# Kernel optimization log

Measured on AMD Instinct MI355X. Metric: run time of the kernel, lower is better.

Reference implementation:

```python
import jax, jax.numpy as jnp
import numpy as np

B, N, M, K, S, P, H, W = 8, 32, 32, 3, 1, 1, 192, 192
NH = (H + 2 * P - K) // S + 1
NW = (W + 2 * P - K) // S + 1


def setup_inputs() -> dict:
    key = jax.random.key(0)
    ks = jax.random.split(key, 8)
    f = lambda k, sh, sc: jax.random.normal(k, sh, jnp.float32) * sc
    return {
        "x": f(ks[0], (B, N, H, W), 1.0),
        "a1_w": f(ks[1], (K * K, N, K, K), 0.05),  # attention1 conv k x k
        "a1_b": jnp.zeros((K * K,), jnp.float32),
        "a2_w": f(ks[2], (K * K, K * K), 0.1),      # attention1 1x1 conv
        "a2_b": jnp.zeros((K * K,), jnp.float32),
        "a3_w": f(ks[3], (K * K, K * K), 0.1),      # attention1 1x1 conv
        "a3_b": jnp.zeros((K * K,), jnp.float32),
        "b1_w": f(ks[4], (M, N), 0.05),             # attention3 1x1 conv
        "b1_b": jnp.zeros((M,), jnp.float32),
        "b2_w": f(ks[5], (M, M), 0.05),             # attention3 1x1 conv
        "b2_b": jnp.zeros((M,), jnp.float32),
        "weight": f(ks[6], (M, N, K, K), 0.05),     # main conv weight
    }


def _attention1(x, a1_w, a1_b, a2_w, a2_b, a3_w, a3_b):
    # Conv(k) -> ReLU -> Conv1x1 -> ReLU -> Conv1x1 -> Sigmoid; out [B, K*K, NH, NW]
    a = jax.lax.conv_general_dilated(
        x, a1_w, (S, S), [(P, P), (P, P)],
        dimension_numbers=("NCHW", "OIHW", "NCHW"))
    a = jax.nn.relu(a + a1_b[None, :, None, None])
    a = jax.nn.relu(jnp.einsum("oi,bihw->bohw", a2_w, a) + a2_b[None, :, None, None])
    a = jnp.einsum("oi,bihw->bohw", a3_w, a) + a3_b[None, :, None, None]
    return jax.nn.sigmoid(a)


def _unfold(x):
    # torch F.unfold ordering: channel-major, kernel positions inner.
    # returns [B, N, K*K, NH, NW]
    xp = jnp.pad(x, ((0, 0), (0, 0), (P, P), (P, P)))
    cols = [xp[:, :, i:i + (NH - 1) * S + 1:S, j:j + (NW - 1) * S + 1:S]
            for i in range(K) for j in range(K)]
    return jnp.stack(cols, axis=2)


def reference(x, a1_w, a1_b, a2_w, a2_b, a3_w, a3_b, b1_w, b1_b, b2_w, b2_b, weight):
    att = _attention1(x, a1_w, a1_b, a2_w, a2_b, a3_w, a3_b)  # [B, K*K, NH, NW]
    pat = _unfold(x)                                          # [B, N, K*K, NH, NW]
    w = weight.reshape(M, N, K * K)
    # attention-weighted unfold + matmul + fold, fused as one einsum
    y = jnp.einsum("bnphw,bphw,mnp->bmhw", pat, att, w)       # [B, M, NH, NW]
    # attention3 bias: global avg pool -> 1x1 -> ReLU -> 1x1
    pooled = x.mean(axis=(2, 3))                              # [B, N]
    h = jax.nn.relu(pooled @ b1_w.T + b1_b)
    bias = h @ b2_w.T + b2_b                                  # [B, M]
    return y + bias[:, :, None, None]
```

## Files before the change

### kernel.cpp

```cpp
#include <hip/hip_runtime.h>
#include <math.h>

#define B_ 8
#define N_ 32
#define M_ 32
#define HW 192

typedef __attribute__((ext_vector_type(8))) short short8;
typedef __attribute__((ext_vector_type(4))) float float4_;

__device__ inline unsigned short f2bf(float f) {
    unsigned int b = __float_as_uint(f);
    b += 0x7FFF + ((b >> 16) & 1);
    return (unsigned short)(b >> 16);
}
__device__ inline float bf2f(unsigned short u) {
    return __uint_as_float((unsigned int)u << 16);
}

union U8 { short8 s; unsigned int u[4]; };

__global__ __launch_bounds__(256) void pool_prep_kernel(
    const float* __restrict__ x, const float* __restrict__ a1w,
    const float* __restrict__ weight, float* __restrict__ pooled,
    unsigned short* __restrict__ a1A, unsigned short* __restrict__ wA) {
    if (blockIdx.x == 256) {
        int tid = threadIdx.x;
        for (int idx = tid; idx < 9 * 512; idx += 256) {
            int j = idx & 7, l = (idx >> 3) & 63, c = idx >> 9;
            int o = l & 15, n = (l >> 4) * 8 + j;
            float v = (o < 9) ? a1w[(o * N_ + n) * 9 + c] : 0.f;
            a1A[idx] = f2bf(v);
        }
        for (int idx = tid; idx < 9 * 1024; idx += 256) {
            int j = idx & 7, l = (idx >> 3) & 63, mt = (idx >> 9) & 1, c = idx >> 10;
            int m = mt * 16 + (l & 15), n = (l >> 4) * 8 + j;
            wA[idx] = f2bf(weight[(m * N_ + n) * 9 + c]);
        }
        return;
    }
    int bn = blockIdx.x;
    const float4_* p = (const float4_*)(x + (size_t)bn * (HW * HW));
    float s = 0.f;
    for (int i = threadIdx.x; i < (HW * HW) / 4; i += 256) {
        float4_ v = p[i];
        s += (v[0] + v[1]) + (v[2] + v[3]);
    }
#pragma unroll
    for (int off = 32; off > 0; off >>= 1) s += __shfl_down(s, off, 64);
    __shared__ float red[4];
    if ((threadIdx.x & 63) == 0) red[threadIdx.x >> 6] = s;
    __syncthreads();
    if (threadIdx.x == 0)
        pooled[bn] = (red[0] + red[1] + red[2] + red[3]) * (1.f / (HW * HW));
}

__global__ __launch_bounds__(256) void laconv_kernel(
    const float* __restrict__ x, const float* __restrict__ a1b,
    const float* __restrict__ a2w, const float* __restrict__ a2b,
    const float* __restrict__ a3w, const float* __restrict__ a3b,
    const unsigned short* __restrict__ a1A, const unsigned short* __restrict__ wA,
    const float* __restrict__ pooled, const float* __restrict__ b1w,
    const float* __restrict__ b1b, const float* __restrict__ b2w,
    const float* __restrict__ b2b, float* __restrict__ out) {
    __shared__ __align__(16) unsigned short xs[324 * 40];
    __shared__ unsigned short att_s[9 * 264];
    __shared__ float hsh[M_];
    __shared__ __align__(16) float bias_lds[M_];

    const int id = blockIdx.x;
    const int b = id & 7;
    const int t = id >> 3;
    const int bx = t % 12, by = t / 12;
    const int th0 = by * 16, tw0 = bx * 16;
    const int tid = threadIdx.x;
    const int wv = tid >> 6, lane = tid & 63;
    const int tx = lane & 15, ks = lane >> 4;
    const float* xb = x + (size_t)b * N_ * HW * HW;

    float fv[5][8];
    int posv[5], grpv[5];
#pragma unroll
    for (int it0 = 0; it0 < 5; ++it0) {
        int it = tid + it0 * 256;
        int grp = it / 324;
        int pos = it - grp * 324;
        posv[it0] = pos; grpv[it0] = grp;
        int r = pos / 18, cc = pos - r * 18;
        int h = th0 + r - 1, wc = tw0 + cc - 1;
        const float* src = xb + (size_t)(grp * 8) * (HW * HW) + h * HW + wc;
        if (((unsigned)h < HW) && ((unsigned)wc < HW)) {
#pragma unroll
            for (int i = 0; i < 8; ++i) fv[it0][i] = src[i * (HW * HW)];
        } else {
#pragma unroll
            for (int i = 0; i < 8; ++i) fv[it0][i] = 0.f;
        }
    }
    float fr[8];
    int posr = 0;
    if (tid < 16) {
        int it = 1280 + tid;
        int pos = it - 3 * 324;
        posr = pos;
        int r = pos / 18, cc = pos - r * 18;
        int h = th0 + r - 1, wc = tw0 + cc - 1;
        const float* src = xb + (size_t)24 * (HW * HW) + h * HW + wc;
        if (((unsigned)h < HW) && ((unsigned)wc < HW)) {
#pragma unroll
            for (int i = 0; i < 8; ++i) fr[i] = src[i * (HW * HW)];
        } else {
#pragma unroll
            for (int i = 0; i < 8; ++i) fr[i] = 0.f;
        }
    }
#pragma unroll
    for (int it0 = 0; it0 < 5; ++it0) {
        U8 tt;
#pragma unroll
        for (int i = 0; i < 4; ++i)
            tt.u[i] = (unsigned)f2bf(fv[it0][2 * i]) |
                      ((unsigned)f2bf(fv[it0][2 * i + 1]) << 16);
        *(short8*)&xs[posv[it0] * 40 + grpv[it0] * 8] = tt.s;
    }
    if (tid < 16) {
        U8 tt;
#pragma unroll
        for (int i = 0; i < 4; ++i)
            tt.u[i] = (unsigned)f2bf(fr[2 * i]) | ((unsigned)f2bf(fr[2 * i + 1]) << 16);
        *(short8*)&xs[posr * 40 + 24] = tt.s;
    }
    if (tid < M_) {
        float s = b1b[tid];
#pragma unroll
        for (int n = 0; n < N_; n++) s += pooled[b * N_ + n] * b1w[tid * N_ + n];
        hsh[tid] = fmaxf(s, 0.f);
    }
    __syncthreads();
    if (tid < M_) {
        float s2 = b2b[tid];
#pragma unroll
        for (int q = 0; q < M_; q++) s2 += hsh[q] * b2w[tid * M_ + q];
        bias_lds[tid] = s2;
    }

    const int pb = (wv * 4) * 720 + tx * 40 + ks * 8;
    const float4_ zero4 = {0.f, 0.f, 0.f, 0.f};

    float4_ aacc[4];
#pragma unroll
    for (int g = 0; g < 4; ++g) aacc[g] = zero4;
#pragma unroll
    for (int c = 0; c < 9; ++c) {
        short8 aA = ((const short8*)a1A)[c * 64 + lane];
        const int coff = (c / 3) * 720 + (c % 3) * 40;
#pragma unroll
        for (int g = 0; g < 4; ++g) {
            short8 bP = *(const short8*)&xs[pb + g * 720 + coff];
            aacc[g] = __builtin_amdgcn_mfma_f32_16x16x32_bf16(aA, bP, aacc[g], 0, 0, 0);
        }
    }
#pragma unroll
    for (int g = 0; g < 4; ++g) {
#pragma unroll
        for (int reg = 0; reg < 4; ++reg) {
            int o = ks * 4 + reg;
            if (o < 9) att_s[o * 264 + (wv * 4 + g) * 16 + tx] = f2bf(aacc[g][reg]);
        }
    }
    __syncthreads();

    float t1[9], t2[9], attv[9];
#pragma unroll
    for (int o = 0; o < 9; ++o)
        t1[o] = fmaxf(bf2f(att_s[o * 264 + tid]) + a1b[o], 0.f);
#pragma unroll
    for (int o2 = 0; o2 < 9; ++o2) {
        float s = a2b[o2];
#pragma unroll
        for (int o = 0; o < 9; ++o) s += a2w[o2 * 9 + o] * t1[o];
        t2[o2] = fmaxf(s, 0.f);
    }
#pragma unroll
    for (int o3 = 0; o3 < 9; ++o3) {
        float s = a3b[o3];
#pragma unroll
        for (int o2 = 0; o2 < 9; ++o2) s += a3w[o3 * 9 + o2] * t2[o2];
        attv[o3] = 1.f / (1.f + __expf(-s));
    }
#pragma unroll
    for (int p = 0; p < 9; ++p) att_s[p * 264 + tid] = f2bf(attv[p]);
    __syncthreads();

    float4_ acc0[4], acc1[4];
#pragma unroll
    for (int g = 0; g < 4; ++g) { acc0[g] = zero4; acc1[g] = zero4; }
#pragma unroll
    for (int c = 0; c < 9; ++c) {
        short8 w0 = ((const short8*)wA)[c * 128 + lane];
        short8 w1 = ((const short8*)wA)[c * 128 + 64 + lane];
        const int coff = (c / 3) * 720 + (c % 3) * 40;
#pragma unroll
        for (int g = 0; g < 4; ++g) {
            short8 bP = *(const short8*)&xs[pb + g * 720 + coff];
            float av = bf2f(att_s[c * 264 + (wv * 4 + g) * 16 + tx]);
            float4_ av4 = {av, av, av, av};
            float4_ z0 = __builtin_amdgcn_mfma_f32_16x16x32_bf16(w0, bP, zero4, 0, 0, 0);
            float4_ z1 = __builtin_amdgcn_mfma_f32_16x16x32_bf16(w1, bP, zero4, 0, 0, 0);
            acc0[g] = acc0[g] + av4 * z0;
            acc1[g] = acc1[g] + av4 * z1;
        }
    }

    const int wc = tw0 + tx;
    float4_ bv0 = *(const float4_*)&bias_lds[ks * 4];
    float4_ bv1 = *(const float4_*)&bias_lds[16 + ks * 4];
#pragma unroll
    for (int g = 0; g < 4; ++g) {
        int h = th0 + wv * 4 + g;
#pragma unroll
        for (int reg = 0; reg < 4; ++reg) {
            int m0 = ks * 4 + reg;
            out[((b * M_ + m0) * HW + h) * HW + wc] = acc0[g][reg] + bv0[reg];
            out[((b * M_ + m0 + 16) * HW + h) * HW + wc] = acc1[g][reg] + bv1[reg];
        }
    }
}

extern "C" void kernel_launch(void* const* d_in, const int* in_sizes, int n_in,
                              void* d_out, int out_size, void* d_ws,
                              size_t ws_size, hipStream_t stream) {
    const float* x   = (const float*)d_in[0];
    const float* a1w = (const float*)d_in[1];
    const float* a1b = (const float*)d_in[2];
    const float* a2w = (const float*)d_in[3];
    const float* a2b = (const float*)d_in[4];
    const float* a3w = (const float*)d_in[5];
    const float* a3b = (const float*)d_in[6];
    const float* b1w = (const float*)d_in[7];
    const float* b1b = (const float*)d_in[8];
    const float* b2w = (const float*)d_in[9];
    const float* b2b = (const float*)d_in[10];
    const float* wgt = (const float*)d_in[11];
    float* out = (float*)d_out;

    char* ws = (char*)d_ws;
    float* pooled        = (float*)(ws);
    unsigned short* a1A  = (unsigned short*)(ws + 2048);
    unsigned short* wAf  = (unsigned short*)(ws + 11264);

    pool_prep_kernel<<<dim3(B_ * N_ + 1), dim3(256), 0, stream>>>(
        x, a1w, wgt, pooled, a1A, wAf);
    laconv_kernel<<<dim3(12 * 12 * B_), dim3(256), 0, stream>>>(
        x, a1b, a2w, a2b, a3w, a3b, a1A, wAf, pooled, b1w, b1b, b2w, b2b, out);
    (void)in_sizes; (void)n_in; (void)out_size; (void)ws_size;
}
```

Measured before the change: 145.0 us.

## Pre-convert input to channels-last bf16 buffer before main conv kernel

```diff
diff --git a/kernel.cpp b/kernel.cpp
--- a/kernel.cpp
+++ b/kernel.cpp
@@ -5,6 +5,9 @@
 #define N_ 32
 #define M_ 32
 #define HW 192
+#define NPIX (HW * HW)
+#define CONV_BLKS (B_ * 144)
+#define POOL_BLKS (B_ * N_)
 
 typedef __attribute__((ext_vector_type(8))) short short8;
 typedef __attribute__((ext_vector_type(4))) float float4_;
@@ -20,43 +23,64 @@
 
 union U8 { short8 s; unsigned int u[4]; };
 
-__global__ __launch_bounds__(256) void pool_prep_kernel(
+__global__ __launch_bounds__(256) void convert_pool_prep(
     const float* __restrict__ x, const float* __restrict__ a1w,
     const float* __restrict__ weight, float* __restrict__ pooled,
-    unsigned short* __restrict__ a1A, unsigned short* __restrict__ wA) {
-    if (blockIdx.x == 256) {
-        int tid = threadIdx.x;
-        for (int idx = tid; idx < 9 * 512; idx += 256) {
-            int j = idx & 7, l = (idx >> 3) & 63, c = idx >> 9;
-            int o = l & 15, n = (l >> 4) * 8 + j;
-            float v = (o < 9) ? a1w[(o * N_ + n) * 9 + c] : 0.f;
-            a1A[idx] = f2bf(v);
-        }
-        for (int idx = tid; idx < 9 * 1024; idx += 256) {
-            int j = idx & 7, l = (idx >> 3) & 63, mt = (idx >> 9) & 1, c = idx >> 10;
-            int m = mt * 16 + (l & 15), n = (l >> 4) * 8 + j;
-            wA[idx] = f2bf(weight[(m * N_ + n) * 9 + c]);
+    unsigned short* __restrict__ a1A, unsigned short* __restrict__ wA,
+    unsigned short* __restrict__ xbf) {
+    const int id = blockIdx.x, tid = threadIdx.x;
+    if (id < CONV_BLKS) {
+        const int b = id / 144, chunk = id - b * 144;
+        const int pix = chunk * 256 + tid;
+        const float* src = x + (size_t)b * N_ * NPIX + pix;
+        float v[32];
+#pragma unroll
+        for (int n = 0; n < N_; ++n) v[n] = src[(size_t)n * NPIX];
+        U8 tt;
+        unsigned short* dst = xbf + ((size_t)b * NPIX + pix) * 32;
+#pragma unroll
+        for (int q = 0; q < 4; ++q) {
+#pragma unroll
+            for (int i = 0; i < 4; ++i)
+                tt.u[i] = (unsigned)f2bf(v[q * 8 + 2 * i]) |
+                          ((unsigned)f2bf(v[q * 8 + 2 * i + 1]) << 16);
+            *(short8*)(dst + q * 8) = tt.s;
         }
         return;
     }
-    int bn = blockIdx.x;
-    const float4_* p = (const float4_*)(x + (size_t)bn * (HW * HW));
-    float s = 0.f;
-    for (int i = threadIdx.x; i < (HW * HW) / 4; i += 256) {
-        float4_ v = p[i];
-        s += (v[0] + v[1]) + (v[2] + v[3]);
-    }
-#pragma unroll
-    for (int off = 32; off > 0; off >>= 1) s += __shfl_down(s, off, 64);
-    __shared__ float red[4];
-    if ((threadIdx.x & 63) == 0) red[threadIdx.x >> 6] = s;
-    __syncthreads();
-    if (threadIdx.x == 0)
-        pooled[bn] = (red[0] + red[1] + red[2] + red[3]) * (1.f / (HW * HW));
+    if (id < CONV_BLKS + POOL_BLKS) {
+        const int bn = id - CONV_BLKS;
+        const float4_* p = (const float4_*)(x + (size_t)bn * NPIX);
+        float s = 0.f;
+        for (int i = tid; i < NPIX / 4; i += 256) {
+            float4_ v = p[i];
+            s += (v[0] + v[1]) + (v[2] + v[3]);
+        }
+#pragma unroll
+        for (int off = 32; off > 0; off >>= 1) s += __shfl_down(s, off, 64);
+        __shared__ float red[4];
+        if ((tid & 63) == 0) red[tid >> 6] = s;
+        __syncthreads();
+        if (tid == 0)
+            pooled[bn] = (red[0] + red[1] + red[2] + red[3]) * (1.f / NPIX);
+        return;
+    }
+    const int c = id - (CONV_BLKS + POOL_BLKS);
+    for (int idx = tid; idx < 512; idx += 256) {
+        int j = idx & 7, l = idx >> 3;
+        int o = l & 15, n = (l >> 4) * 8 + j;
+        float v = (o < 9) ? a1w[(o * N_ + n) * 9 + c] : 0.f;
+        a1A[c * 512 + idx] = f2bf(v);
+    }
+    for (int idx = tid; idx < 1024; idx += 256) {
+        int j = idx & 7, l = (idx >> 3) & 63, mt = idx >> 9;
+        int m = mt * 16 + (l & 15), n = (l >> 4) * 8 + j;
+        wA[c * 1024 + idx] = f2bf(weight[(m * N_ + n) * 9 + c]);
+    }
 }
 
 __global__ __launch_bounds__(256) void laconv_kernel(
-    const float* __restrict__ x, const float* __restrict__ a1b,
+    const unsigned short* __restrict__ xbf, const float* __restrict__ a1b,
     const float* __restrict__ a2w, const float* __restrict__ a2b,
     const float* __restrict__ a3w, const float* __restrict__ a3b,
     const unsigned short* __restrict__ a1A, const unsigned short* __restrict__ wA,
@@ -76,60 +100,38 @@
     const int tid = threadIdx.x;
     const int wv = tid >> 6, lane = tid & 63;
     const int tx = lane & 15, ks = lane >> 4;
-    const float* xb = x + (size_t)b * N_ * HW * HW;
-
-    float fv[5][8];
-    int posv[5], grpv[5];
+    const unsigned short* xb = xbf + (size_t)b * NPIX * 32;
+
+    short8 sv[5];
+    int pv[5];
 #pragma unroll
     for (int it0 = 0; it0 < 5; ++it0) {
         int it = tid + it0 * 256;
-        int grp = it / 324;
-        int pos = it - grp * 324;
-        posv[it0] = pos; grpv[it0] = grp;
+        int pos = it >> 2, grp = it & 3;
+        pv[it0] = pos * 40 + grp * 8;
         int r = pos / 18, cc = pos - r * 18;
         int h = th0 + r - 1, wc = tw0 + cc - 1;
-        const float* src = xb + (size_t)(grp * 8) * (HW * HW) + h * HW + wc;
         if (((unsigned)h < HW) && ((unsigned)wc < HW)) {
-#pragma unroll
-            for (int i = 0; i < 8; ++i) fv[it0][i] = src[i * (HW * HW)];
+            sv[it0] = *(const short8*)(xb + ((size_t)(h * HW + wc)) * 32 + grp * 8);
         } else {
-#pragma unroll
-            for (int i = 0; i < 8; ++i) fv[it0][i] = 0.f;
-        }
-    }
-    float fr[8];
-    int posr = 0;
+            sv[it0] = (short8)0;
+        }
+    }
+    short8 svr = (short8)0;
+    int pvr = 0;
     if (tid < 16) {
         int it = 1280 + tid;
-        int pos = it - 3 * 324;
-        posr = pos;
+        int pos = it >> 2, grp = it & 3;
+        pvr = pos * 40 + grp * 8;
         int r = pos / 18, cc = pos - r * 18;
         int h = th0 + r - 1, wc = tw0 + cc - 1;
-        const float* src = xb + (size_t)24 * (HW * HW) + h * HW + wc;
-        if (((unsigned)h < HW) && ((unsigned)wc < HW)) {
-#pragma unroll
-            for (int i = 0; i < 8; ++i) fr[i] = src[i * (HW * HW)];
-        } else {
-#pragma unroll
-            for (int i = 0; i < 8; ++i) fr[i] = 0.f;
-        }
-    }
-#pragma unroll
-    for (int it0 = 0; it0 < 5; ++it0) {
-        U8 tt;
-#pragma unroll
-        for (int i = 0; i < 4; ++i)
-            tt.u[i] = (unsigned)f2bf(fv[it0][2 * i]) |
-                      ((unsigned)f2bf(fv[it0][2 * i + 1]) << 16);
-        *(short8*)&xs[posv[it0] * 40 + grpv[it0] * 8] = tt.s;
-    }
-    if (tid < 16) {
-        U8 tt;
-#pragma unroll
-        for (int i = 0; i < 4; ++i)
-            tt.u[i] = (unsigned)f2bf(fr[2 * i]) | ((unsigned)f2bf(fr[2 * i + 1]) << 16);
-        *(short8*)&xs[posr * 40 + 24] = tt.s;
-    }
+        if (((unsigned)h < HW) && ((unsigned)wc < HW))
+            svr = *(const short8*)(xb + ((size_t)(h * HW + wc)) * 32 + grp * 8);
+    }
+#pragma unroll
+    for (int it0 = 0; it0 < 5; ++it0) *(short8*)&xs[pv[it0]] = sv[it0];
+    if (tid < 16) *(short8*)&xs[pvr] = svr;
+
     if (tid < M_) {
         float s = b1b[tid];
 #pragma unroll
@@ -248,10 +250,11 @@
     float* pooled        = (float*)(ws);
     unsigned short* a1A  = (unsigned short*)(ws + 2048);
     unsigned short* wAf  = (unsigned short*)(ws + 11264);
-
-    pool_prep_kernel<<<dim3(B_ * N_ + 1), dim3(256), 0, stream>>>(
-        x, a1w, wgt, pooled, a1A, wAf);
+    unsigned short* xbf  = (unsigned short*)(ws + 32768);
+
+    convert_pool_prep<<<dim3(CONV_BLKS + POOL_BLKS + 9), dim3(256), 0, stream>>>(
+        x, a1w, wgt, pooled, a1A, wAf, xbf);
     laconv_kernel<<<dim3(12 * 12 * B_), dim3(256), 0, stream>>>(
-        x, a1b, a2w, a2b, a3w, a3b, a1A, wAf, pooled, b1w, b1b, b2w, b2b, out);
+        xbf, a1b, a2w, a2b, a3w, a3b, a1A, wAf, pooled, b1w, b1b, b2w, b2b, out);
     (void)in_sizes; (void)n_in; (void)out_size; (void)ws_size;
 }
```

After: 145.0 us. About the same (+0.0%).
